# Optimization experiments

Hardware: AMD Instinct MI355X
Metric: run time of the kernel (lower is better)

Reference implementation:

```python
import jax, jax.numpy as jnp
import numpy as np

N_ENTITIES = 500000
N_RELATIONS = 16
DIM = 64
N_HOP = 2
BATCH = 256
N_MEMORY = 32


def setup_inputs() -> dict:
    key = jax.random.key(0)
    k1, k2, k3, k4, k5, k6 = jax.random.split(key, 6)
    entity_emb = jax.random.normal(k1, (N_ENTITIES + 1, DIM), dtype=jnp.float32) * 0.02
    relation_emb = jax.random.normal(k2, (N_RELATIONS, DIM), dtype=jnp.float32) * 0.02
    items = jax.random.randint(k3, (BATCH,), 0, N_ENTITIES)
    shape = (N_HOP, BATCH, N_RELATIONS, N_MEMORY)
    memories_h = jax.random.randint(k4, shape, 0, N_ENTITIES)
    memories_r = jax.random.randint(k5, shape, 0, N_RELATIONS)
    memories_t = jax.random.randint(k6, shape, 0, N_ENTITIES)
    return {
        "entity_emb": entity_emb,
        "relation_emb": relation_emb,
        "items": items,
        "memories_h": memories_h,
        "memories_r": memories_r,
        "memories_t": memories_t,
    }


def reference(entity_emb, relation_emb, items, memories_h, memories_r, memories_t):
    # items_emb / v: [B, D]
    v = entity_emb[items]

    def per_hop(mh, mr, mt):
        # gathers: [B, R, M, D]
        h = entity_emb[mh]
        r = relation_emb[mr]
        t = entity_emb[mt]
        # relation-modulated head: Rh = r * h  -> [B, R, M, D]
        Rh = r * h
        # attention scores against item embedding v: [B, R, M]
        scores = jnp.einsum("brmd,bd->brm", Rh, v)
        probs = jax.nn.softmax(scores, axis=-1)
        # weighted sum of tail embeddings: [B, R, D]
        return jnp.einsum("brmd,brm->brd", t, probs)

    # vmap over hop axis -> o: [n_hop, B, R, D]
    o = jax.vmap(per_hop)(memories_h, memories_r, memories_t)
    return o
```

## Files before the change

kernel.cpp:

```cpp
#include <hip/hip_runtime.h>
#include <hip/hip_bf16.h>

constexpr int BATCH = 256;
constexpr int NREL  = 16;
constexpr int DIM   = 64;
constexpr int NHOP  = 2;
constexpr int NMEM  = 32;

__global__ __launch_bounds__(256)
void kgan_kernel(const float* __restrict__ ent,
                 const float* __restrict__ rel,
                 const int*   __restrict__ items,
                 const int*   __restrict__ mh,
                 const int*   __restrict__ mr,
                 const int*   __restrict__ mt,
                 float*       __restrict__ out)
{
    __shared__ float rel_lds[NREL * DIM];
    {
        const int t = threadIdx.x;
        reinterpret_cast<float4*>(rel_lds)[t] =
            reinterpret_cast<const float4*>(rel)[t];
    }
    __syncthreads();

    const int gtid = blockIdx.x * blockDim.x + threadIdx.x;
    const int wave = gtid >> 6;
    const int lane = threadIdx.x & 63;

    const int b = (wave >> 4) & (BATCH - 1);

    const int item = items[b];
    const float v = ent[(size_t)item * DIM + lane];

    const int base = wave * NMEM;
    const int lm   = lane & 31;
    const int vh   = mh[base + lm];
    const int vr   = mr[base + lm];
    const int vt   = mt[base + lm];

    float hb[NMEM], tb[NMEM];
    #pragma unroll
    for (int m = 0; m < NMEM; ++m) {
        const int hid = __shfl(vh, m, 64);
        hb[m] = ent[(size_t)hid * DIM + lane];
    }
    #pragma unroll
    for (int m = 0; m < NMEM; ++m) {
        const int tid = __shfl(vt, m, 64);
        tb[m] = ent[(size_t)tid * DIM + lane];
    }

    float scp[NMEM / 2];
    const bool hi = (lane & 32) != 0;
    #pragma unroll
    for (int j = 0; j < NMEM / 2; ++j) {
        const int r0 = __shfl(vr, 2 * j, 64);
        const int r1 = __shfl(vr, 2 * j + 1, 64);
        float a = hb[2 * j]     * rel_lds[r0 * DIM + lane] * v;
        float c = hb[2 * j + 1] * rel_lds[r1 * DIM + lane] * v;
        a += __shfl_xor(a, 32, 64);
        c += __shfl_xor(c, 32, 64);
        float p = hi ? c : a;
        #pragma unroll
        for (int off = 16; off >= 1; off >>= 1)
            p += __shfl_xor(p, off, 64);
        scp[j] = p;
    }

    float mx = scp[0];
    #pragma unroll
    for (int j = 1; j < NMEM / 2; ++j) mx = fmaxf(mx, scp[j]);
    mx = fmaxf(mx, __shfl_xor(mx, 32, 64));

    float sum = 0.f;
    #pragma unroll
    for (int j = 0; j < NMEM / 2; ++j) {
        scp[j] = __expf(scp[j] - mx);
        sum += scp[j];
    }
    sum += __shfl_xor(sum, 32, 64);
    const float inv = 1.f / sum;

    float o = 0.f;
    #pragma unroll
    for (int j = 0; j < NMEM / 2; ++j) {
        const float pc = scp[j] * inv;
        const float po = __shfl_xor(pc, 32, 64);
        const float te = tb[2 * j], to_ = tb[2 * j + 1];
        const float t1 = hi ? to_ : te;
        const float t2 = hi ? te  : to_;
        o = fmaf(pc, t1, o);
        o = fmaf(po, t2, o);
    }

    out[(size_t)wave * DIM + lane] = o;
}

extern "C" void kernel_launch(void* const* d_in, const int* in_sizes, int n_in,
                              void* d_out, int out_size, void* d_ws, size_t ws_size,
                              hipStream_t stream) {
    const float* ent   = (const float*)d_in[0];
    const float* rel   = (const float*)d_in[1];
    const int*   items = (const int*)d_in[2];
    const int*   mh    = (const int*)d_in[3];
    const int*   mr    = (const int*)d_in[4];
    const int*   mt    = (const int*)d_in[5];
    float* out = (float*)d_out;

    const int total_waves = NHOP * BATCH * NREL;
    const int threads = 256;
    const int blocks = total_waves * 64 / threads;

    kgan_kernel<<<blocks, threads, 0, stream>>>(ent, rel, items, mh, mr, mt, out);
}
```

Before: 29.30 us.

## Remap wave lanes so each 16-lane group gathers whole rows with float4 loads

Each wave now splits its 64 lanes into four 16-lane groups. Each group loads one full 64-float entity row per memory slot using float4 loads, so every lane handles four dims of four memories at once. This replaces 64 scalar gather loads per lane with 16 vector loads and cuts the shuffles needed for the score reductions. The cost is a cross-group shuffle reduction of the output accumulator, a final store from only one quarter of the lanes, and more register pressure from the float4 buffers.

```diff
diff --git a/kernel.cpp b/kernel.cpp
--- a/kernel.cpp
+++ b/kernel.cpp
@@ -27,11 +27,13 @@
     const int gtid = blockIdx.x * blockDim.x + threadIdx.x;
     const int wave = gtid >> 6;
     const int lane = threadIdx.x & 63;
+    const int sub  = lane >> 4;
+    const int q    = lane & 15;
 
     const int b = (wave >> 4) & (BATCH - 1);
 
     const int item = items[b];
-    const float v = ent[(size_t)item * DIM + lane];
+    const float4 v4 = reinterpret_cast<const float4*>(ent)[(size_t)item * 16 + q];
 
     const int base = wave * NMEM;
     const int lm   = lane & 31;
@@ -39,62 +41,76 @@
     const int vr   = mr[base + lm];
     const int vt   = mt[base + lm];
 
-    float hb[NMEM], tb[NMEM];
+    const float4* ent4 = reinterpret_cast<const float4*>(ent);
+    const float4* rl4  = reinterpret_cast<const float4*>(rel_lds);
+
+    float4 hb[8], tb[8];
+    int ridx[8];
     #pragma unroll
-    for (int m = 0; m < NMEM; ++m) {
-        const int hid = __shfl(vh, m, 64);
-        hb[m] = ent[(size_t)hid * DIM + lane];
+    for (int j = 0; j < 8; ++j) {
+        const int hid = __shfl(vh, 4 * j + sub, 64);
+        hb[j] = ent4[(size_t)hid * 16 + q];
     }
     #pragma unroll
-    for (int m = 0; m < NMEM; ++m) {
-        const int tid = __shfl(vt, m, 64);
-        tb[m] = ent[(size_t)tid * DIM + lane];
+    for (int j = 0; j < 8; ++j) {
+        const int tid = __shfl(vt, 4 * j + sub, 64);
+        tb[j] = ent4[(size_t)tid * 16 + q];
+    }
+    #pragma unroll
+    for (int j = 0; j < 8; ++j)
+        ridx[j] = __shfl(vr, 4 * j + sub, 64);
+
+    float sc[8];
+    #pragma unroll
+    for (int j = 0; j < 8; ++j) {
+        const float4 r4 = rl4[ridx[j] * 16 + q];
+        const float4 h4 = hb[j];
+        float p = h4.x * r4.x * v4.x;
+        p = fmaf(h4.y * r4.y, v4.y, p);
+        p = fmaf(h4.z * r4.z, v4.z, p);
+        p = fmaf(h4.w * r4.w, v4.w, p);
+        #pragma unroll
+        for (int off = 8; off >= 1; off >>= 1)
+            p += __shfl_xor(p, off, 64);
+        sc[j] = p;
     }
 
-    float scp[NMEM / 2];
-    const bool hi = (lane & 32) != 0;
+    float mx = sc[0];
     #pragma unroll
-    for (int j = 0; j < NMEM / 2; ++j) {
-        const int r0 = __shfl(vr, 2 * j, 64);
-        const int r1 = __shfl(vr, 2 * j + 1, 64);
-        float a = hb[2 * j]     * rel_lds[r0 * DIM + lane] * v;
-        float c = hb[2 * j + 1] * rel_lds[r1 * DIM + lane] * v;
-        a += __shfl_xor(a, 32, 64);
-        c += __shfl_xor(c, 32, 64);
-        float p = hi ? c : a;
-        #pragma unroll
-        for (int off = 16; off >= 1; off >>= 1)
-            p += __shfl_xor(p, off, 64);
-        scp[j] = p;
-    }
-
-    float mx = scp[0];
-    #pragma unroll
-    for (int j = 1; j < NMEM / 2; ++j) mx = fmaxf(mx, scp[j]);
+    for (int j = 1; j < 8; ++j) mx = fmaxf(mx, sc[j]);
+    mx = fmaxf(mx, __shfl_xor(mx, 16, 64));
     mx = fmaxf(mx, __shfl_xor(mx, 32, 64));
 
     float sum = 0.f;
     #pragma unroll
-    for (int j = 0; j < NMEM / 2; ++j) {
-        scp[j] = __expf(scp[j] - mx);
-        sum += scp[j];
+    for (int j = 0; j < 8; ++j) {
+        sc[j] = __expf(sc[j] - mx);
+        sum += sc[j];
     }
+    sum += __shfl_xor(sum, 16, 64);
     sum += __shfl_xor(sum, 32, 64);
     const float inv = 1.f / sum;
 
-    float o = 0.f;
+    float4 acc = make_float4(0.f, 0.f, 0.f, 0.f);
     #pragma unroll
-    for (int j = 0; j < NMEM / 2; ++j) {
-        const float pc = scp[j] * inv;
-        const float po = __shfl_xor(pc, 32, 64);
-        const float te = tb[2 * j], to_ = tb[2 * j + 1];
-        const float t1 = hi ? to_ : te;
-        const float t2 = hi ? te  : to_;
-        o = fmaf(pc, t1, o);
-        o = fmaf(po, t2, o);
+    for (int j = 0; j < 8; ++j) {
+        const float p = sc[j] * inv;
+        acc.x = fmaf(p, tb[j].x, acc.x);
+        acc.y = fmaf(p, tb[j].y, acc.y);
+        acc.z = fmaf(p, tb[j].z, acc.z);
+        acc.w = fmaf(p, tb[j].w, acc.w);
     }
+    acc.x += __shfl_xor(acc.x, 16, 64);
+    acc.y += __shfl_xor(acc.y, 16, 64);
+    acc.z += __shfl_xor(acc.z, 16, 64);
+    acc.w += __shfl_xor(acc.w, 16, 64);
+    acc.x += __shfl_xor(acc.x, 32, 64);
+    acc.y += __shfl_xor(acc.y, 32, 64);
+    acc.z += __shfl_xor(acc.z, 32, 64);
+    acc.w += __shfl_xor(acc.w, 32, 64);
 
-    out[(size_t)wave * DIM + lane] = o;
+    if (sub == 0)
+        reinterpret_cast<float4*>(out)[(size_t)wave * 16 + q] = acc;
 }
 
 extern "C" void kernel_launch(void* const* d_in, const int* in_sizes, int n_in,
```

Result: faster. 25.35 us (-13.5%).
